# Optimization experiments

Measured on AMD Instinct MI355X. Metric: run time of the kernel, lower is better.

The kernel has to match this reference:

```python
import jax, jax.numpy as jnp
import numpy as np

B, L, C, D = 4, 2048, 64, 4


def setup_inputs() -> dict:
    key = jax.random.key(0)
    k1, k2, k3, k4 = jax.random.split(key, 4)
    # |A| kept < ~0.92 so the length-2048 recurrence stays bounded
    A_re = jax.random.uniform(k1, (B, L, C, D), jnp.float32, -0.65, 0.65)
    A_im = jax.random.uniform(k2, (B, L, C, D), jnp.float32, -0.65, 0.65)
    X_re = jax.random.normal(k3, (B, L, C, D, D), jnp.float32)
    X_im = jax.random.normal(k4, (B, L, C, D, D), jnp.float32)
    return {"A_re": A_re, "A_im": A_im, "X_re": X_re, "X_im": X_im}


def _combine(c1, c2):
    # first-order linear recurrence combine: (a, x) o (b, y) = (b*a, b*x + y)
    a1, x1 = c1
    a2, x2 = c2
    return a2 * a1, a2 * x1 + x2


def reference(A_re, A_im, X_re, X_im):
    # Diagonal complex pscan: Y[t] = A[t] * Y[t-1] + X[t], elementwise,
    # with diagonal A [B,L,C,D] broadcast over the trailing D dim of X [B,L,C,D,D]
    A = (A_re + 1j * A_im).astype(jnp.complex64)[..., None]  # [B,L,C,D,1]
    X = (X_re + 1j * X_im).astype(jnp.complex64)             # [B,L,C,D,D]
    _, Y = jax.lax.associative_scan(_combine, (A, X), axis=1)
    # return real view [B,L,C,D,D,2] (real, imag) like torch.view_as_real
    return jnp.stack([Y.real, Y.imag], axis=-1)
```

## Files before the change

kernel.cpp:

```cpp
#include <hip/hip_runtime.h>

#define BB 4
#define LL 2048
#define CC 64
#define DD 4
#define NN (CC * DD * DD)
#define AN (CC * DD)
#define TPB 1024
#define N4PB 4
#define NSEGS (TPB / N4PB)
#define TT (LL / NSEGS)

typedef float f32x4 __attribute__((ext_vector_type(4)));

__global__ __launch_bounds__(1024, 4) void pscan_onepass4(
    const float* __restrict__ A_re, const float* __restrict__ A_im,
    const f32x4* __restrict__ X_re4, const f32x4* __restrict__ X_im4,
    f32x4* __restrict__ out4) {
  const int sid = (blockIdx.x & 7) * 32 + (blockIdx.x >> 3);
  const int b    = sid >> 6;
  const int n4g  = sid & 63;
  const int tid  = threadIdx.x;
  const int n4l  = tid & (N4PB - 1);
  const int tseg = tid >> 2;
  const int n4   = n4g * N4PB + n4l;
  const int t0   = tseg * TT;
  const int base = (b * LL + t0) * AN + n4;

  float ar[TT], ai[TT];
  f32x4 xr[TT], xi[TT];
  float p_re = 1.f, p_im = 0.f;
  float s_re[4] = {0.f, 0.f, 0.f, 0.f};
  float s_im[4] = {0.f, 0.f, 0.f, 0.f};
#pragma unroll
  for (int t = 0; t < TT; ++t) {
    const float are = A_re[base + t * AN];
    const float aim = A_im[base + t * AN];
    ar[t] = are; ai[t] = aim;
    xr[t] = X_re4[base + t * AN];
    xi[t] = X_im4[base + t * AN];
    const float npre = are * p_re - aim * p_im;
    const float npim = are * p_im + aim * p_re;
    p_re = npre; p_im = npim;
#pragma unroll
    for (int j = 0; j < 4; ++j) {
      const float nsre = are * s_re[j] - aim * s_im[j] + xr[t][j];
      const float nsim = are * s_im[j] + aim * s_re[j] + xi[t][j];
      s_re[j] = nsre; s_im[j] = nsim;
    }
  }

  __shared__ float lds[TPB * 11];
  const int q = tid * 11;
  lds[q + 0] = p_re; lds[q + 1] = p_im;
#pragma unroll
  for (int j = 0; j < 4; ++j) { lds[q + 2 + j] = s_re[j]; lds[q + 6 + j] = s_im[j]; }

  float vp_re = p_re, vp_im = p_im;
  float vs_re[4], vs_im[4];
#pragma unroll
  for (int j = 0; j < 4; ++j) { vs_re[j] = s_re[j]; vs_im[j] = s_im[j]; }

  for (int d = 1; d < NSEGS; d <<= 1) {
    __syncthreads();
    float wp_re = 1.f, wp_im = 0.f;
    float ws_re[4] = {0.f, 0.f, 0.f, 0.f};
    float ws_im[4] = {0.f, 0.f, 0.f, 0.f};
    if (tseg >= d) {
      const int q2 = q - d * (N4PB * 11);
      wp_re = lds[q2 + 0]; wp_im = lds[q2 + 1];
#pragma unroll
      for (int j = 0; j < 4; ++j) { ws_re[j] = lds[q2 + 2 + j]; ws_im[j] = lds[q2 + 6 + j]; }
    }
    __syncthreads();
    if (tseg >= d) {
      const float np_re = vp_re * wp_re - vp_im * wp_im;
      const float np_im = vp_re * wp_im + vp_im * wp_re;
#pragma unroll
      for (int j = 0; j < 4; ++j) {
        const float ns_re = vp_re * ws_re[j] - vp_im * ws_im[j] + vs_re[j];
        const float ns_im = vp_re * ws_im[j] + vp_im * ws_re[j] + vs_im[j];
        vs_re[j] = ns_re; vs_im[j] = ns_im;
      }
      vp_re = np_re; vp_im = np_im;
      lds[q + 0] = vp_re; lds[q + 1] = vp_im;
#pragma unroll
      for (int j = 0; j < 4; ++j) { lds[q + 2 + j] = vs_re[j]; lds[q + 6 + j] = vs_im[j]; }
    }
  }
  __syncthreads();

  float y_re[4] = {0.f, 0.f, 0.f, 0.f};
  float y_im[4] = {0.f, 0.f, 0.f, 0.f};
  if (tseg > 0) {
    const int qc = q - N4PB * 11;
#pragma unroll
    for (int j = 0; j < 4; ++j) { y_re[j] = lds[qc + 2 + j]; y_im[j] = lds[qc + 6 + j]; }
  }

  const int ob = (b * LL + t0) * (2 * AN) + n4 * 2;
#pragma unroll
  for (int t = 0; t < TT; ++t) {
    const float are = ar[t], aim = ai[t];
#pragma unroll
    for (int j = 0; j < 4; ++j) {
      const float ny_re = are * y_re[j] - aim * y_im[j] + xr[t][j];
      const float ny_im = are * y_im[j] + aim * y_re[j] + xi[t][j];
      y_re[j] = ny_re; y_im[j] = ny_im;
    }
    f32x4 o0 = {y_re[0], y_im[0], y_re[1], y_im[1]};
    f32x4 o1 = {y_re[2], y_im[2], y_re[3], y_im[3]};
    out4[ob + t * (2 * AN)]     = o0;
    out4[ob + t * (2 * AN) + 1] = o1;
  }
}

extern "C" void kernel_launch(void* const* d_in, const int* in_sizes, int n_in,
                              void* d_out, int out_size, void* d_ws, size_t ws_size,
                              hipStream_t stream) {
  const float* A_re  = (const float*)d_in[0];
  const float* A_im  = (const float*)d_in[1];
  const f32x4* X_re4 = (const f32x4*)d_in[2];
  const f32x4* X_im4 = (const f32x4*)d_in[3];
  f32x4* out4 = (f32x4*)d_out;
  (void)d_ws; (void)ws_size;

  const int blocks = BB * (AN / N4PB);
  pscan_onepass4<<<blocks, TPB, 0, stream>>>(A_re, A_im, X_re4, X_im4, out4);
}
```

Before: 155.1 us.

## Write local scan results early and fix up with carry via prefix products

Rather than keeping all A and X values in registers until the carry is known, the kernel now writes the local (zero-carry) scan to the output during the first pass and stores only the running products of A per step. After the cross-segment scan, each thread re-reads its output, adds prefix-product times carry, and writes it back. This cuts register pressure (the launch bound min-blocks hint is also dropped) at the price of an extra read and write of the output through global memory or cache.

```diff
diff --git a/kernel.cpp b/kernel.cpp
--- a/kernel.cpp
+++ b/kernel.cpp
@@ -4,7 +4,6 @@
 #define LL 2048
 #define CC 64
 #define DD 4
-#define NN (CC * DD * DD)
 #define AN (CC * DD)
 #define TPB 1024
 #define N4PB 4
@@ -13,7 +12,7 @@
 
 typedef float f32x4 __attribute__((ext_vector_type(4)));
 
-__global__ __launch_bounds__(1024, 4) void pscan_onepass4(
+__global__ __launch_bounds__(TPB) void pscan_onepass6(
     const float* __restrict__ A_re, const float* __restrict__ A_im,
     const f32x4* __restrict__ X_re4, const f32x4* __restrict__ X_im4,
     f32x4* __restrict__ out4) {
@@ -26,9 +25,9 @@
   const int n4   = n4g * N4PB + n4l;
   const int t0   = tseg * TT;
   const int base = (b * LL + t0) * AN + n4;
+  const int ob   = (b * LL + t0) * (2 * AN) + n4 * 2;
 
-  float ar[TT], ai[TT];
-  f32x4 xr[TT], xi[TT];
+  float pp_re[TT], pp_im[TT];
   float p_re = 1.f, p_im = 0.f;
   float s_re[4] = {0.f, 0.f, 0.f, 0.f};
   float s_im[4] = {0.f, 0.f, 0.f, 0.f};
@@ -36,18 +35,22 @@
   for (int t = 0; t < TT; ++t) {
     const float are = A_re[base + t * AN];
     const float aim = A_im[base + t * AN];
-    ar[t] = are; ai[t] = aim;
-    xr[t] = X_re4[base + t * AN];
-    xi[t] = X_im4[base + t * AN];
+    const f32x4 xr = X_re4[base + t * AN];
+    const f32x4 xi = X_im4[base + t * AN];
     const float npre = are * p_re - aim * p_im;
     const float npim = are * p_im + aim * p_re;
     p_re = npre; p_im = npim;
+    pp_re[t] = p_re; pp_im[t] = p_im;
 #pragma unroll
     for (int j = 0; j < 4; ++j) {
-      const float nsre = are * s_re[j] - aim * s_im[j] + xr[t][j];
-      const float nsim = are * s_im[j] + aim * s_re[j] + xi[t][j];
+      const float nsre = are * s_re[j] - aim * s_im[j] + xr[j];
+      const float nsim = are * s_im[j] + aim * s_re[j] + xi[j];
       s_re[j] = nsre; s_im[j] = nsim;
     }
+    f32x4 o0 = {s_re[0], s_im[0], s_re[1], s_im[1]};
+    f32x4 o1 = {s_re[2], s_im[2], s_re[3], s_im[3]};
+    out4[ob + t * (2 * AN)]     = o0;
+    out4[ob + t * (2 * AN) + 1] = o1;
   }
 
   __shared__ float lds[TPB * 11];
@@ -90,28 +93,27 @@
   }
   __syncthreads();
 
-  float y_re[4] = {0.f, 0.f, 0.f, 0.f};
-  float y_im[4] = {0.f, 0.f, 0.f, 0.f};
   if (tseg > 0) {
     const int qc = q - N4PB * 11;
+    float cy_re[4], cy_im[4];
 #pragma unroll
-    for (int j = 0; j < 4; ++j) { y_re[j] = lds[qc + 2 + j]; y_im[j] = lds[qc + 6 + j]; }
-  }
-
-  const int ob = (b * LL + t0) * (2 * AN) + n4 * 2;
+    for (int j = 0; j < 4; ++j) { cy_re[j] = lds[qc + 2 + j]; cy_im[j] = lds[qc + 6 + j]; }
 #pragma unroll
-  for (int t = 0; t < TT; ++t) {
-    const float are = ar[t], aim = ai[t];
-#pragma unroll
-    for (int j = 0; j < 4; ++j) {
-      const float ny_re = are * y_re[j] - aim * y_im[j] + xr[t][j];
-      const float ny_im = are * y_im[j] + aim * y_re[j] + xi[t][j];
-      y_re[j] = ny_re; y_im[j] = ny_im;
+    for (int t = 0; t < TT; ++t) {
+      f32x4 o0 = out4[ob + t * (2 * AN)];
+      f32x4 o1 = out4[ob + t * (2 * AN) + 1];
+      const float wr = pp_re[t], wi = pp_im[t];
+      o0.x += wr * cy_re[0] - wi * cy_im[0];
+      o0.y += wr * cy_im[0] + wi * cy_re[0];
+      o0.z += wr * cy_re[1] - wi * cy_im[1];
+      o0.w += wr * cy_im[1] + wi * cy_re[1];
+      o1.x += wr * cy_re[2] - wi * cy_im[2];
+      o1.y += wr * cy_im[2] + wi * cy_re[2];
+      o1.z += wr * cy_re[3] - wi * cy_im[3];
+      o1.w += wr * cy_im[3] + wi * cy_re[3];
+      out4[ob + t * (2 * AN)]     = o0;
+      out4[ob + t * (2 * AN) + 1] = o1;
     }
-    f32x4 o0 = {y_re[0], y_im[0], y_re[1], y_im[1]};
-    f32x4 o1 = {y_re[2], y_im[2], y_re[3], y_im[3]};
-    out4[ob + t * (2 * AN)]     = o0;
-    out4[ob + t * (2 * AN) + 1] = o1;
   }
 }
 
@@ -126,5 +128,5 @@
   (void)d_ws; (void)ws_size;
 
   const int blocks = BB * (AN / N4PB);
-  pscan_onepass4<<<blocks, TPB, 0, stream>>>(A_re, A_im, X_re4, X_im4, out4);
+  pscan_onepass6<<<blocks, TPB, 0, stream>>>(A_re, A_im, X_re4, X_im4, out4);
 }
```

Result: slower. 173.8 us (+12.1%).
